# Optimization experiments

Measured on AMD Instinct MI355X. Metric: run time of the kernel, lower is better.

Reference implementation:

```python
import jax, jax.numpy as jnp
import numpy as np

D, H, B, NSTEPS = 128, 512, 128, 16


def setup_inputs() -> dict:
    key = jax.random.key(0)
    k0, k1, k2, k3 = jax.random.split(key, 4)
    s1 = 1.0 / np.sqrt(D)
    s2 = 0.1 / np.sqrt(H)  # small output scale keeps the flow well-conditioned
    return {
        "x0": jax.random.normal(k0, (B, D), jnp.float32),
        "W1": jax.random.normal(k1, (D, H), jnp.float32) * s1,
        "b1": jnp.zeros((H,), jnp.float32),
        "u1": jax.random.normal(k2, (H,), jnp.float32) * 0.1,
        "W2": jax.random.normal(k3, (H, D), jnp.float32) * s2,
        "b2": jnp.zeros((D,), jnp.float32),
        "n_steps": NSTEPS,
    }


def reference(x0, W1, b1, u1, W2, b2, n_steps):
    d = x0.shape[-1]
    LOG2PI = float(np.log(2.0 * np.pi))
    # log prob of x0 under standard-normal prior p0
    log_px0 = -0.5 * jnp.sum(x0 * x0, axis=-1) - 0.5 * d * LOG2PI
    dt = 1.0 / n_steps

    sg = jax.lax.stop_gradient
    W1s, b1s, u1s, W2s, b2s = sg(W1), sg(b1), sg(u1), sg(W2), sg(b2)

    def vf(t, x, w1, c1, v1, w2, c2):  # time-conditioned MLP vector field, x: (d,)
        return jnp.tanh(x @ w1 + c1 + t * v1) @ w2 + c2

    eye = jnp.eye(d, dtype=x0.dtype)

    def f_single(t, x):
        # exact Jacobian trace via vmapped JVP over identity tangents (stop-grad params)
        apply_sg = lambda xx: vf(t, xx, W1s, b1s, u1s, W2s, b2s)
        jvp1 = lambda e: jax.jvp(apply_sg, (x,), (e,))[1]
        jac = jax.vmap(jvp1)(eye)              # (d, d)
        dxdt = vf(t, x, W1, b1, u1, W2, b2)    # with grad-carrying params
        dlogpxdt = -jnp.trace(jac)
        gradlogpx = -x                          # grad log of standard-normal target
        dkldt = -jnp.vdot(gradlogpx, dxdt) + dlogpxdt
        return dxdt, dlogpxdt, dkldt

    rhs = jax.vmap(f_single, in_axes=(None, 0))  # batch over samples

    # Dopri5 Butcher tableau (fixed-step 5th-order solution)
    A = (
        (1 / 5,),
        (3 / 40, 9 / 40),
        (44 / 45, -56 / 15, 32 / 9),
        (19372 / 6561, -25360 / 2187, 64448 / 6561, -212 / 729),
        (9017 / 3168, -355 / 33, 46732 / 5247, 49 / 176, -5103 / 18656),
    )
    C = (1 / 5, 3 / 10, 4 / 5, 8 / 9, 1.0)
    BW = (35 / 384, 0.0, 500 / 1113, 125 / 192, -2187 / 6784, 11 / 84)

    def lin(y, ks, cs):  # y + dt * sum(c_i * k_i), tree-structured state
        return jax.tree_util.tree_map(
            lambda yv, *kv: yv + dt * sum(c * k for c, k in zip(cs, kv)), y, *ks)

    def step(y, t):
        ks = [rhs(t, y[0])]
        for ai, ci in zip(A, C):
            yi = lin(y, ks, ai)
            ks.append(rhs(t + ci * dt, yi[0]))
        return lin(y, ks, BW), None

    nb = x0.shape[0]
    y0 = (x0, jnp.zeros((nb,), x0.dtype), jnp.zeros((nb,), x0.dtype))
    ts = jnp.arange(n_steps, dtype=x0.dtype) * dt
    (z, log_det, kl), _ = jax.lax.scan(step, y0, ts)
    log_px = log_px0 + log_det
    return z, log_px, kl
```

## Files before the change

### kernel.cpp

```cpp
#include <hip/hip_runtime.h>

#define TPB 512

typedef _Float16 hf2 __attribute__((ext_vector_type(2)));

__device__ __forceinline__ hf2 as_h2(unsigned u) { return __builtin_bit_cast(hf2, u); }
__device__ __forceinline__ unsigned pk2h(float a, float b) {
    unsigned la = (unsigned)__builtin_bit_cast(unsigned short, (_Float16)a);
    unsigned hb = (unsigned)__builtin_bit_cast(unsigned short, (_Float16)b);
    return la | (hb << 16);
}
__device__ __forceinline__ unsigned short h16(float a) {
    return __builtin_bit_cast(unsigned short, (_Float16)a);
}
#define FDOT2(w, x, acc) __builtin_amdgcn_fdot2(as_h2(w), as_h2(x), (acc), false)

#define G16(M) M(0) M(1) M(2) M(3) M(4) M(5) M(6) M(7) M(8) M(9) M(10) M(11) \
  M(12) M(13) M(14) M(15)

#define RED64(v) { v += __shfl_xor(v,32,64); v += __shfl_xor(v,16,64); \
  v += __shfl_xor(v,8,64); v += __shfl_xor(v,4,64); v += __shfl_xor(v,2,64); \
  v += __shfl_xor(v,1,64); }

__global__ __launch_bounds__(TPB, 1) void vi_node_kernel(
    const float* __restrict__ x0, const float* __restrict__ W1,
    const float* __restrict__ b1, const float* __restrict__ u1,
    const float* __restrict__ W2, const float* __restrict__ b2,
    const int* __restrict__ nsp, float* __restrict__ out, int nB)
{
    const int s    = blockIdx.x;
    const int t    = threadIdx.x;
    const int j    = t & 127;
    const int q    = t >> 7;
    const int kb   = q << 7;
    const int lane = t & 63;
    const int wid  = t >> 6;

    __shared__ uint4 W1L[16 * 512];
    __shared__ __align__(16) float    xs32[128];
    __shared__ __align__(16) unsigned xshU[64];
    __shared__ __align__(16) float    ys[128];
    __shared__ __align__(16) unsigned aLhU[256];
    __shared__ __align__(16) float    part[4][128];
    __shared__ __align__(16) float    kx[6][128];
    __shared__ float wredT[2][6][8];
    __shared__ float wredX[2][6][2];
    __shared__ float sqred[2];

#pragma unroll
    for (int c = 0; c < 16; ++c) {
        const float* gp = W1 + (8 * c) * 512 + t;
        uint4 wv;
        wv.x = pk2h(gp[0],        gp[512]);
        wv.y = pk2h(gp[2 * 512],  gp[3 * 512]);
        wv.z = pk2h(gp[4 * 512],  gp[5 * 512]);
        wv.w = pk2h(gp[6 * 512],  gp[7 * 512]);
        W1L[c * 512 + t] = wv;
    }

#define DECLZ(g) unsigned z_##g##_0, z_##g##_1, z_##g##_2, z_##g##_3;
    G16(DECLZ)
#define PKW2(r) pk2h(W2[(r) * 128 + j], W2[((r) + 1) * 128 + j])
#define LOADZ(g) { const int r_ = kb + 8 * (g); \
    z_##g##_0 = PKW2(r_);     z_##g##_1 = PKW2(r_ + 2); \
    z_##g##_2 = PKW2(r_ + 4); z_##g##_3 = PKW2(r_ + 6); }
    G16(LOADZ)

    const float b1k = b1[t];
    const float u1k = u1[t];
    const float b2j = b2[j];

    const int ns = nsp[0];
    const float dt = 1.f / (float)ns;

    if (t < 128) {
        float xv = x0[s * 128 + t];
        ys[t] = xv;
        xs32[t] = xv;
        ((unsigned short*)xshU)[t] = h16(xv);
        float sq = xv * xv;
        RED64(sq)
        if (lane == 0) sqred[wid] = sq;
    }
    __syncthreads();

    float wd = 0.f;
    {
        const float4* w2r4 = (const float4*)(W2 + t * 128);
#pragma unroll
        for (int c = 0; c < 16; ++c) {
            uint4 wv = W1L[c * 512 + t];
            float4 a4 = w2r4[2 * c], b4 = w2r4[2 * c + 1];
            wd = FDOT2(wv.x, pk2h(a4.x, a4.y), wd);
            wd = FDOT2(wv.y, pk2h(a4.z, a4.w), wd);
            wd = FDOT2(wv.z, pk2h(b4.x, b4.y), wd);
            wd = FDOT2(wv.w, pk2h(b4.z, b4.w), wd);
        }
    }
    const float sumsq = sqred[0] + sqred[1];
    float ld_acc = 0.f, kl_acc = 0.f;

#define H8(c) { uint4 w_ = W1L[(c) * 512 + t]; \
    const uint4 xv_ = *(const uint4*)&xshU[(c) * 4]; \
    m0 = FDOT2(w_.x, xv_.x, m0); m1 = FDOT2(w_.y, xv_.y, m1); \
    m2 = FDOT2(w_.z, xv_.z, m2); m3 = FDOT2(w_.w, xv_.w, m3); }

#define P8(g) { const uint4 av_ = *(const uint4*)&aLhU[q * 64 + (g) * 4]; \
    p0 = FDOT2(z_##g##_0, av_.x, p0); p1 = FDOT2(z_##g##_1, av_.y, p1); \
    p2 = FDOT2(z_##g##_2, av_.z, p2); p3 = FDOT2(z_##g##_3, av_.w, p3); }

#define K(sidx) kx[sidx][t]

#define EVAL(STAGE, TVAL, XNEW, EXTRA)                                         \
    {                                                                          \
        float m0 = 0.f, m1 = 0.f, m2 = 0.f, m3 = 0.f;                          \
        H8(0) H8(1) H8(2) H8(3) H8(4) H8(5) H8(6) H8(7)                        \
        H8(8) H8(9) H8(10) H8(11) H8(12) H8(13) H8(14) H8(15)                  \
        float hh = fmaf((TVAL), u1k, b1k) + ((m0 + m1) + (m2 + m3));           \
        float ee = __expf(2.f * hh);                                           \
        float aa = 1.f - 2.f / (ee + 1.f);                           \
        ((unsigned short*)aLhU)[t] = h16(aa);                                  \
        float trp = (1.f - aa * aa) * wd;                                      \
        RED64(trp)                                                             \
        if (lane == 0) wredT[par][STAGE][wid] = trp;                           \
        __syncthreads();                             \
        float p0 = 0.f, p1 = 0.f, p2 = 0.f, p3 = 0.f;                          \
        P8(0) P8(1) P8(2) P8(3) P8(4) P8(5) P8(6) P8(7)                        \
        P8(8) P8(9) P8(10) P8(11) P8(12) P8(13) P8(14) P8(15)                  \
        part[q][j] = (p0 + p1) + (p2 + p3);                                    \
        __syncthreads();                               \
        if (t < 128) {                                                         \
            float dx = ((part[0][t] + part[1][t]) + (part[2][t] + part[3][t])) \
                       + b2j;                                                  \
            kx[STAGE][t] = dx;                                                 \
            float xd = xs32[t] * dx;                                           \
            RED64(xd)                                                          \
            if (lane == 0) wredX[par][STAGE][wid] = xd;                        \
            float xnew = (XNEW);                                               \
            xs32[t] = xnew;                                                    \
            ((unsigned short*)xshU)[t] = h16(xnew);                            \
            EXTRA                                                              \
        }                                                                      \
        __syncthreads();                               \
    }

    for (int n = 0; n < ns; ++n) {
        const float tn = (float)n;
        const int par = n & 1;

        EVAL(0, dt * tn,
             fmaf(dt, 0.2f * dx, ys[t]), ;)

        EVAL(1, dt * (tn + 0.2f),
             ys[t] + dt * (0.075f * K(0) + 0.225f * dx), ;)

        EVAL(2, dt * (tn + 0.3f),
             ys[t] + dt * ((float)(44.0/45.0)  * K(0) + (float)(-56.0/15.0) * K(1)
                         + (float)(32.0/9.0)   * dx), ;)

        EVAL(3, dt * (tn + 0.8f),
             ys[t] + dt * ((float)(19372.0/6561.0) * K(0) + (float)(-25360.0/2187.0) * K(1)
                         + (float)(64448.0/6561.0) * K(2) + (float)(-212.0/729.0)    * dx), ;)

        EVAL(4, dt * (tn + (float)(8.0/9.0)),
             ys[t] + dt * ((float)(9017.0/3168.0)  * K(0) + (float)(-355.0/33.0)     * K(1)
                         + (float)(46732.0/5247.0) * K(2) + (float)(49.0/176.0)      * K(3)
                         + (float)(-5103.0/18656.0)* dx), ;)

        EVAL(5, dt * (tn + 1.0f),
             ys[t] + dt * ((float)(35.0/384.0)     * K(0) + (float)(500.0/1113.0)   * K(2)
                         + (float)(125.0/192.0)    * K(3) + (float)(-2187.0/6784.0) * K(4)
                         + (float)(11.0/84.0)      * dx),
             ys[t] = xnew;)

        if (t == 0) {
#define TAILS(sidx, bw) { \
            float tr_ = ((wredT[par][sidx][0] + wredT[par][sidx][1])  \
                       + (wredT[par][sidx][2] + wredT[par][sidx][3])) \
                      + ((wredT[par][sidx][4] + wredT[par][sidx][5])  \
                       + (wredT[par][sidx][6] + wredT[par][sidx][7])); \
            float dv_ = wredX[par][sidx][0] + wredX[par][sidx][1]; \
            ld_acc += dt * (bw) * (-tr_); \
            kl_acc += dt * (bw) * (dv_ - tr_); }
            TAILS(0, (float)(35.0/384.0))
            TAILS(2, (float)(500.0/1113.0))
            TAILS(3, (float)(125.0/192.0))
            TAILS(4, (float)(-2187.0/6784.0))
            TAILS(5, (float)(11.0/84.0))
        }
    }

    if (t < 128) out[s * 128 + t] = ys[t];
    if (t == 0) {
        const float LOG2PI = 1.8378770664093454f;
        float lpx0 = -0.5f * sumsq - 0.5f * 128.f * LOG2PI;
        out[nB * 128 + s]      = lpx0 + ld_acc;
        out[nB * 128 + nB + s] = kl_acc;
    }
}

extern "C" void kernel_launch(void* const* d_in, const int* in_sizes, int n_in,
                              void* d_out, int out_size, void* d_ws, size_t ws_size,
                              hipStream_t stream) {
    const float* x0 = (const float*)d_in[0];
    const float* W1 = (const float*)d_in[1];
    const float* b1 = (const float*)d_in[2];
    const float* u1 = (const float*)d_in[3];
    const float* W2 = (const float*)d_in[4];
    const float* b2 = (const float*)d_in[5];
    const int*  nsp = (const int*)d_in[6];
    float* out = (float*)d_out;
    const int nB = in_sizes[0] / 128;

    hipLaunchKernelGGL(vi_node_kernel, dim3(nB), dim3(TPB), 0, stream,
                       x0, W1, b1, u1, W2, b2, nsp, out, nB);
}
```

Before: 232.8 us.

## Hold W1/W2 in registers across 1024 threads with DPP/swizzle reductions

Doubles the block to 1024 threads and keeps both weight matrices as packed fp16 in registers, dropping the shared-memory W1 tile. Each thread handles two hidden units (W1 pass) and two output columns (W2 pass), with partial dot products reduced by DPP and swizzle lane ops in place of the shared-memory partials buffer. Integration state and the trace and KL accumulators stay in registers, and their block reductions are deferred to the end, which removes the per-step tail on thread 0. The tradeoff is heavy register pressure and more redundant per-lane arithmetic in exchange for less LDS traffic and fewer serial reduction steps.

Result: slower. 262.6 us (+12.8%).

```diff
diff --git a/kernel.cpp b/kernel.cpp
--- a/kernel.cpp
+++ b/kernel.cpp
@@ -1,6 +1,6 @@
 #include <hip/hip_runtime.h>
 
-#define TPB 512
+#define TPB 1024
 
 typedef _Float16 hf2 __attribute__((ext_vector_type(2)));
 
@@ -10,17 +10,21 @@
     unsigned hb = (unsigned)__builtin_bit_cast(unsigned short, (_Float16)b);
     return la | (hb << 16);
 }
-__device__ __forceinline__ unsigned short h16(float a) {
-    return __builtin_bit_cast(unsigned short, (_Float16)a);
-}
 #define FDOT2(w, x, acc) __builtin_amdgcn_fdot2(as_h2(w), as_h2(x), (acc), false)
 
-#define G16(M) M(0) M(1) M(2) M(3) M(4) M(5) M(6) M(7) M(8) M(9) M(10) M(11) \
-  M(12) M(13) M(14) M(15)
+#define DPPADD(v, CTRL) ((v) + __int_as_float(__builtin_amdgcn_update_dpp( \
+    0, __float_as_int(v), (CTRL), 0xF, 0xF, false)))
+#define SWZADD(v, OFF) ((v) + __int_as_float(__builtin_amdgcn_ds_swizzle( \
+    __float_as_int(v), (OFF))))
+#define RED4(v)  { v = DPPADD(v, 0xB1); v = DPPADD(v, 0x4E); }
+#define RED16(v) { v = DPPADD(v, 0xB1); v = DPPADD(v, 0x4E); \
+                   v = SWZADD(v, 0x101F); v = DPPADD(v, 0x128); }
 
 #define RED64(v) { v += __shfl_xor(v,32,64); v += __shfl_xor(v,16,64); \
   v += __shfl_xor(v,8,64); v += __shfl_xor(v,4,64); v += __shfl_xor(v,2,64); \
   v += __shfl_xor(v,1,64); }
+
+#define G4(M) M(0) M(1) M(2) M(3)
 
 __global__ __launch_bounds__(TPB, 1) void vi_node_kernel(
     const float* __restrict__ x0, const float* __restrict__ W1,
@@ -28,174 +32,178 @@
     const float* __restrict__ W2, const float* __restrict__ b2,
     const int* __restrict__ nsp, float* __restrict__ out, int nB)
 {
-    const int s    = blockIdx.x;
-    const int t    = threadIdx.x;
-    const int j    = t & 127;
-    const int q    = t >> 7;
-    const int kb   = q << 7;
-    const int lane = t & 63;
-    const int wid  = t >> 6;
-
-    __shared__ uint4 W1L[16 * 512];
-    __shared__ __align__(16) float    xs32[128];
-    __shared__ __align__(16) unsigned xshU[64];
-    __shared__ __align__(16) float    ys[128];
-    __shared__ __align__(16) unsigned aLhU[256];
-    __shared__ __align__(16) float    part[4][128];
-    __shared__ __align__(16) float    kx[6][128];
-    __shared__ float wredT[2][6][8];
-    __shared__ float wredX[2][6][2];
-    __shared__ float sqred[2];
-
+    const int s  = blockIdx.x;
+    const int t  = threadIdx.x;
+    const int l  = t & 63;
+    const int w  = t >> 6;
+    const int rg    = l & 3;
+    const int cpair = 16 * w + (l >> 2);
+    const int c0 = 2 * cpair, c1 = c0 + 1;
+    const int rg4   = l & 15;
+    const int jpair = 4 * w + (l >> 4);
+    const int j0 = 2 * jpair, j1 = j0 + 1;
+
+    __shared__ __align__(16) unsigned xsPK[64];
+    __shared__ __align__(16) unsigned aPKp[320];
+    __shared__ float redA[16], redB[16], sqred[2];
+
+#define DECLW(cc) unsigned wA##cc##_0, wA##cc##_1, wA##cc##_2, wA##cc##_3, \
+                           wB##cc##_0, wB##cc##_1, wB##cc##_2, wB##cc##_3; \
+                  unsigned zA##cc##_0, zA##cc##_1, zA##cc##_2, zA##cc##_3, \
+                           zB##cc##_0, zB##cc##_1, zB##cc##_2, zB##cc##_3;
+    G4(DECLW)
+
+#define LDW1(cc) { const int r_ = 32 * rg + 8 * (cc); \
+    wA##cc##_0 = pk2h(W1[(r_+0)*512+c0], W1[(r_+1)*512+c0]); \
+    wA##cc##_1 = pk2h(W1[(r_+2)*512+c0], W1[(r_+3)*512+c0]); \
+    wA##cc##_2 = pk2h(W1[(r_+4)*512+c0], W1[(r_+5)*512+c0]); \
+    wA##cc##_3 = pk2h(W1[(r_+6)*512+c0], W1[(r_+7)*512+c0]); \
+    wB##cc##_0 = pk2h(W1[(r_+0)*512+c1], W1[(r_+1)*512+c1]); \
+    wB##cc##_1 = pk2h(W1[(r_+2)*512+c1], W1[(r_+3)*512+c1]); \
+    wB##cc##_2 = pk2h(W1[(r_+4)*512+c1], W1[(r_+5)*512+c1]); \
+    wB##cc##_3 = pk2h(W1[(r_+6)*512+c1], W1[(r_+7)*512+c1]); }
+    G4(LDW1)
+
+#define LDW2(cc) { const int r_ = 32 * rg4 + 8 * (cc); \
+    zA##cc##_0 = pk2h(W2[(r_+0)*128+j0], W2[(r_+1)*128+j0]); \
+    zA##cc##_1 = pk2h(W2[(r_+2)*128+j0], W2[(r_+3)*128+j0]); \
+    zA##cc##_2 = pk2h(W2[(r_+4)*128+j0], W2[(r_+5)*128+j0]); \
+    zA##cc##_3 = pk2h(W2[(r_+6)*128+j0], W2[(r_+7)*128+j0]); \
+    zB##cc##_0 = pk2h(W2[(r_+0)*128+j1], W2[(r_+1)*128+j1]); \
+    zB##cc##_1 = pk2h(W2[(r_+2)*128+j1], W2[(r_+3)*128+j1]); \
+    zB##cc##_2 = pk2h(W2[(r_+4)*128+j1], W2[(r_+5)*128+j1]); \
+    zB##cc##_3 = pk2h(W2[(r_+6)*128+j1], W2[(r_+7)*128+j1]); }
+    G4(LDW2)
+
+    float wd0 = 0.f, wd1 = 0.f;
 #pragma unroll
-    for (int c = 0; c < 16; ++c) {
-        const float* gp = W1 + (8 * c) * 512 + t;
-        uint4 wv;
-        wv.x = pk2h(gp[0],        gp[512]);
-        wv.y = pk2h(gp[2 * 512],  gp[3 * 512]);
-        wv.z = pk2h(gp[4 * 512],  gp[5 * 512]);
-        wv.w = pk2h(gp[6 * 512],  gp[7 * 512]);
-        W1L[c * 512 + t] = wv;
-    }
-
-#define DECLZ(g) unsigned z_##g##_0, z_##g##_1, z_##g##_2, z_##g##_3;
-    G16(DECLZ)
-#define PKW2(r) pk2h(W2[(r) * 128 + j], W2[((r) + 1) * 128 + j])
-#define LOADZ(g) { const int r_ = kb + 8 * (g); \
-    z_##g##_0 = PKW2(r_);     z_##g##_1 = PKW2(r_ + 2); \
-    z_##g##_2 = PKW2(r_ + 4); z_##g##_3 = PKW2(r_ + 6); }
-    G16(LOADZ)
-
-    const float b1k = b1[t];
-    const float u1k = u1[t];
-    const float b2j = b2[j];
+    for (int i = 0; i < 32; ++i) {
+        const int r_ = 32 * rg + i;
+        wd0 = fmaf(W1[r_ * 512 + c0], W2[c0 * 128 + r_], wd0);
+        wd1 = fmaf(W1[r_ * 512 + c1], W2[c1 * 128 + r_], wd1);
+    }
+    RED4(wd0) RED4(wd1)
+
+    const float b1k0 = b1[c0], b1k1 = b1[c1];
+    const float u1k0 = u1[c0], u1k1 = u1[c1];
+    const float b2j0 = b2[j0], b2j1 = b2[j1];
 
     const int ns = nsp[0];
     const float dt = 1.f / (float)ns;
 
+    if (t < 64) xsPK[t] = pk2h(x0[s * 128 + 2 * t], x0[s * 128 + 2 * t + 1]);
     if (t < 128) {
         float xv = x0[s * 128 + t];
-        ys[t] = xv;
-        xs32[t] = xv;
-        ((unsigned short*)xshU)[t] = h16(xv);
         float sq = xv * xv;
         RED64(sq)
-        if (lane == 0) sqred[wid] = sq;
-    }
+        if (l == 0) sqred[w] = sq;
+    }
+    float xc0 = x0[s * 128 + j0], xc1 = x0[s * 128 + j1];
+    float yc0 = xc0, yc1 = xc1;
+    float k0_0=0.f,k0_1=0.f,k1_0=0.f,k1_1=0.f,k2_0=0.f,k2_1=0.f,
+          k3_0=0.f,k3_1=0.f,k4_0=0.f,k4_1=0.f;
+    float tr_loc = 0.f, dot_loc = 0.f;
     __syncthreads();
 
-    float wd = 0.f;
-    {
-        const float4* w2r4 = (const float4*)(W2 + t * 128);
-#pragma unroll
-        for (int c = 0; c < 16; ++c) {
-            uint4 wv = W1L[c * 512 + t];
-            float4 a4 = w2r4[2 * c], b4 = w2r4[2 * c + 1];
-            wd = FDOT2(wv.x, pk2h(a4.x, a4.y), wd);
-            wd = FDOT2(wv.y, pk2h(a4.z, a4.w), wd);
-            wd = FDOT2(wv.z, pk2h(b4.x, b4.y), wd);
-            wd = FDOT2(wv.w, pk2h(b4.z, b4.w), wd);
-        }
-    }
-    const float sumsq = sqred[0] + sqred[1];
-    float ld_acc = 0.f, kl_acc = 0.f;
-
-#define H8(c) { uint4 w_ = W1L[(c) * 512 + t]; \
-    const uint4 xv_ = *(const uint4*)&xshU[(c) * 4]; \
-    m0 = FDOT2(w_.x, xv_.x, m0); m1 = FDOT2(w_.y, xv_.y, m1); \
-    m2 = FDOT2(w_.z, xv_.z, m2); m3 = FDOT2(w_.w, xv_.w, m3); }
-
-#define P8(g) { const uint4 av_ = *(const uint4*)&aLhU[q * 64 + (g) * 4]; \
-    p0 = FDOT2(z_##g##_0, av_.x, p0); p1 = FDOT2(z_##g##_1, av_.y, p1); \
-    p2 = FDOT2(z_##g##_2, av_.z, p2); p3 = FDOT2(z_##g##_3, av_.w, p3); }
-
-#define K(sidx) kx[sidx][t]
-
-#define EVAL(STAGE, TVAL, XNEW, EXTRA)                                         \
+#define HM(cc) { const uint4 xq = *(const uint4*)&xsPK[16 * rg + 4 * (cc)]; \
+    a0 = FDOT2(wA##cc##_0, xq.x, a0); a1 = FDOT2(wA##cc##_1, xq.y, a1); \
+    a0 = FDOT2(wA##cc##_2, xq.z, a0); a1 = FDOT2(wA##cc##_3, xq.w, a1); \
+    b0 = FDOT2(wB##cc##_0, xq.x, b0); b1v = FDOT2(wB##cc##_1, xq.y, b1v); \
+    b0 = FDOT2(wB##cc##_2, xq.z, b0); b1v = FDOT2(wB##cc##_3, xq.w, b1v); }
+
+#define PM(cc) { const uint4 aq = *(const uint4*)&aPKp[20 * rg4 + 4 * (cc)]; \
+    p0 = FDOT2(zA##cc##_0, aq.x, p0); p1 = FDOT2(zA##cc##_1, aq.y, p1); \
+    p0 = FDOT2(zA##cc##_2, aq.z, p0); p1 = FDOT2(zA##cc##_3, aq.w, p1); \
+    q0 = FDOT2(zB##cc##_0, aq.x, q0); q1 = FDOT2(zB##cc##_1, aq.y, q1); \
+    q0 = FDOT2(zB##cc##_2, aq.z, q0); q1 = FDOT2(zB##cc##_3, aq.w, q1); }
+
+#define EVAL(CW, TVAL, KST0, KST1, XN0, XN1, LAST)                             \
     {                                                                          \
-        float m0 = 0.f, m1 = 0.f, m2 = 0.f, m3 = 0.f;                          \
-        H8(0) H8(1) H8(2) H8(3) H8(4) H8(5) H8(6) H8(7)                        \
-        H8(8) H8(9) H8(10) H8(11) H8(12) H8(13) H8(14) H8(15)                  \
-        float hh = fmaf((TVAL), u1k, b1k) + ((m0 + m1) + (m2 + m3));           \
-        float ee = __expf(2.f * hh);                                           \
-        float aa = 1.f - 2.f / (ee + 1.f);                           \
-        ((unsigned short*)aLhU)[t] = h16(aa);                                  \
-        float trp = (1.f - aa * aa) * wd;                                      \
-        RED64(trp)                                                             \
-        if (lane == 0) wredT[par][STAGE][wid] = trp;                           \
-        __syncthreads();                             \
-        float p0 = 0.f, p1 = 0.f, p2 = 0.f, p3 = 0.f;                          \
-        P8(0) P8(1) P8(2) P8(3) P8(4) P8(5) P8(6) P8(7)                        \
-        P8(8) P8(9) P8(10) P8(11) P8(12) P8(13) P8(14) P8(15)                  \
-        part[q][j] = (p0 + p1) + (p2 + p3);                                    \
-        __syncthreads();                               \
-        if (t < 128) {                                                         \
-            float dx = ((part[0][t] + part[1][t]) + (part[2][t] + part[3][t])) \
-                       + b2j;                                                  \
-            kx[STAGE][t] = dx;                                                 \
-            float xd = xs32[t] * dx;                                           \
-            RED64(xd)                                                          \
-            if (lane == 0) wredX[par][STAGE][wid] = xd;                        \
-            float xnew = (XNEW);                                               \
-            xs32[t] = xnew;                                                    \
-            ((unsigned short*)xshU)[t] = h16(xnew);                            \
-            EXTRA                                                              \
-        }                                                                      \
-        __syncthreads();                               \
+        float a0=0.f, a1=0.f, b0=0.f, b1v=0.f;                                 \
+        HM(0) HM(1) HM(2) HM(3)                                                \
+        float sA = a0 + a1, sB = b0 + b1v;                                     \
+        RED4(sA) RED4(sB)                           \
+        float h0 = fmaf((TVAL), u1k0, b1k0) + sA;                              \
+        float h1 = fmaf((TVAL), u1k1, b1k1) + sB;                              \
+        float aa0 = 1.f - 2.f / (__expf(2.f * h0) + 1.f);                      \
+        float aa1 = 1.f - 2.f / (__expf(2.f * h1) + 1.f);                      \
+        if (rg == 0)                                                           \
+            aPKp[(cpair >> 4) * 20 + (cpair & 15)] = pk2h(aa0, aa1);           \
+        tr_loc = fmaf((CW), fmaf(-aa0, aa0, 1.f) * wd0                         \
+                          + fmaf(-aa1, aa1, 1.f) * wd1, tr_loc);               \
+        __syncthreads();                                   \
+        float p0=0.f, p1=0.f, q0=0.f, q1=0.f;                                  \
+        PM(0) PM(1) PM(2) PM(3)                                                \
+        float sp = p0 + p1, sq_ = q0 + q1;                                     \
+        RED16(sp) RED16(sq_)                      \
+        float dx0 = sp + b2j0, dx1 = sq_ + b2j1;                               \
+        dot_loc = fmaf((CW), xc0 * dx0 + xc1 * dx1, dot_loc);                  \
+        KST0; KST1;                                                            \
+        xc0 = (XN0); xc1 = (XN1);                                              \
+        if (LAST) { yc0 = xc0; yc1 = xc1; }                                    \
+        if ((l & 15) == 0) xsPK[jpair] = pk2h(xc0, xc1);                       \
+        __syncthreads();                                   \
     }
 
     for (int n = 0; n < ns; ++n) {
         const float tn = (float)n;
-        const int par = n & 1;
-
-        EVAL(0, dt * tn,
-             fmaf(dt, 0.2f * dx, ys[t]), ;)
-
-        EVAL(1, dt * (tn + 0.2f),
-             ys[t] + dt * (0.075f * K(0) + 0.225f * dx), ;)
-
-        EVAL(2, dt * (tn + 0.3f),
-             ys[t] + dt * ((float)(44.0/45.0)  * K(0) + (float)(-56.0/15.0) * K(1)
-                         + (float)(32.0/9.0)   * dx), ;)
-
-        EVAL(3, dt * (tn + 0.8f),
-             ys[t] + dt * ((float)(19372.0/6561.0) * K(0) + (float)(-25360.0/2187.0) * K(1)
-                         + (float)(64448.0/6561.0) * K(2) + (float)(-212.0/729.0)    * dx), ;)
-
-        EVAL(4, dt * (tn + (float)(8.0/9.0)),
-             ys[t] + dt * ((float)(9017.0/3168.0)  * K(0) + (float)(-355.0/33.0)     * K(1)
-                         + (float)(46732.0/5247.0) * K(2) + (float)(49.0/176.0)      * K(3)
-                         + (float)(-5103.0/18656.0)* dx), ;)
-
-        EVAL(5, dt * (tn + 1.0f),
-             ys[t] + dt * ((float)(35.0/384.0)     * K(0) + (float)(500.0/1113.0)   * K(2)
-                         + (float)(125.0/192.0)    * K(3) + (float)(-2187.0/6784.0) * K(4)
-                         + (float)(11.0/84.0)      * dx),
-             ys[t] = xnew;)
-
-        if (t == 0) {
-#define TAILS(sidx, bw) { \
-            float tr_ = ((wredT[par][sidx][0] + wredT[par][sidx][1])  \
-                       + (wredT[par][sidx][2] + wredT[par][sidx][3])) \
-                      + ((wredT[par][sidx][4] + wredT[par][sidx][5])  \
-                       + (wredT[par][sidx][6] + wredT[par][sidx][7])); \
-            float dv_ = wredX[par][sidx][0] + wredX[par][sidx][1]; \
-            ld_acc += dt * (bw) * (-tr_); \
-            kl_acc += dt * (bw) * (dv_ - tr_); }
-            TAILS(0, (float)(35.0/384.0))
-            TAILS(2, (float)(500.0/1113.0))
-            TAILS(3, (float)(125.0/192.0))
-            TAILS(4, (float)(-2187.0/6784.0))
-            TAILS(5, (float)(11.0/84.0))
-        }
-    }
-
-    if (t < 128) out[s * 128 + t] = ys[t];
+
+        EVAL((float)(35.0/384.0), tn * dt, k0_0 = dx0, k0_1 = dx1,
+             fmaf(dt, 0.2f * dx0, yc0), fmaf(dt, 0.2f * dx1, yc1), 0)
+
+        EVAL(0.0f, (tn + 0.2f) * dt, k1_0 = dx0, k1_1 = dx1,
+             yc0 + dt * (0.075f * k0_0 + 0.225f * dx0),
+             yc1 + dt * (0.075f * k0_1 + 0.225f * dx1), 0)
+
+        EVAL((float)(500.0/1113.0), (tn + 0.3f) * dt, k2_0 = dx0, k2_1 = dx1,
+             yc0 + dt * ((float)(44.0/45.0) * k0_0 + (float)(-56.0/15.0) * k1_0
+                       + (float)(32.0/9.0)  * dx0),
+             yc1 + dt * ((float)(44.0/45.0) * k0_1 + (float)(-56.0/15.0) * k1_1
+                       + (float)(32.0/9.0)  * dx1), 0)
+
+        EVAL((float)(125.0/192.0), (tn + 0.8f) * dt, k3_0 = dx0, k3_1 = dx1,
+             yc0 + dt * ((float)(19372.0/6561.0) * k0_0 + (float)(-25360.0/2187.0) * k1_0
+                       + (float)(64448.0/6561.0) * k2_0 + (float)(-212.0/729.0)    * dx0),
+             yc1 + dt * ((float)(19372.0/6561.0) * k0_1 + (float)(-25360.0/2187.0) * k1_1
+                       + (float)(64448.0/6561.0) * k2_1 + (float)(-212.0/729.0)    * dx1), 0)
+
+        EVAL((float)(-2187.0/6784.0), (tn + (float)(8.0/9.0)) * dt, k4_0 = dx0, k4_1 = dx1,
+             yc0 + dt * ((float)(9017.0/3168.0)  * k0_0 + (float)(-355.0/33.0) * k1_0
+                       + (float)(46732.0/5247.0) * k2_0 + (float)(49.0/176.0)  * k3_0
+                       + (float)(-5103.0/18656.0) * dx0),
+             yc1 + dt * ((float)(9017.0/3168.0)  * k0_1 + (float)(-355.0/33.0) * k1_1
+                       + (float)(46732.0/5247.0) * k2_1 + (float)(49.0/176.0)  * k3_1
+                       + (float)(-5103.0/18656.0) * dx1), 0)
+
+        EVAL((float)(11.0/84.0), (tn + 1.0f) * dt, (void)0, (void)0,
+             yc0 + dt * ((float)(35.0/384.0)  * k0_0 + (float)(500.0/1113.0)   * k2_0
+                       + (float)(125.0/192.0) * k3_0 + (float)(-2187.0/6784.0) * k4_0
+                       + (float)(11.0/84.0)   * dx0),
+             yc1 + dt * ((float)(35.0/384.0)  * k0_1 + (float)(500.0/1113.0)   * k2_1
+                       + (float)(125.0/192.0) * k3_1 + (float)(-2187.0/6784.0) * k4_1
+                       + (float)(11.0/84.0)   * dx1), 1)
+    }
+
+    {
+        float tv = tr_loc;  RED64(tv)  if (l == 0) redA[w] = tv;
+        float dv = dot_loc; RED64(dv)  if (l == 0) redB[w] = dv;
+    }
+    __syncthreads();
+
+    if ((l & 15) == 0) {
+        out[s * 128 + j0] = yc0;
+        out[s * 128 + j1] = yc1;
+    }
     if (t == 0) {
+        float TRs = 0.f, DOs = 0.f;
+#pragma unroll
+        for (int ww = 0; ww < 16; ++ww) { TRs += redA[ww]; DOs += redB[ww]; }
+        const float TR = TRs * dt * 0.25f;
+        const float DO = DOs * dt * (1.f / 16.f);
         const float LOG2PI = 1.8378770664093454f;
-        float lpx0 = -0.5f * sumsq - 0.5f * 128.f * LOG2PI;
-        out[nB * 128 + s]      = lpx0 + ld_acc;
-        out[nB * 128 + nB + s] = kl_acc;
+        float lpx0 = -0.5f * (sqred[0] + sqred[1]) - 0.5f * 128.f * LOG2PI;
+        out[nB * 128 + s]      = lpx0 - TR;
+        out[nB * 128 + nB + s] = DO - TR;
     }
 }
 
```
